# Kernel tuning notes

Measured on AMD Instinct MI355X. Metric: run time of the kernel, lower is better.

## Reference

```python
import jax, jax.numpy as jnp
import numpy as np

B, S = 1, 2048
HID, INTER = 4096, 11008
HEADS, HD = 32, 128
GS = 128
EPS = 1e-6
BASE = 10000.0
IMIN, IMAX = -(2**31), 2**31 - 1


def _rope_tables():
    inv_freq = 1.0 / (BASE ** (np.arange(0, HD, 2, dtype=np.float32) / HD))
    t = np.arange(S, dtype=np.float32)
    freqs = np.outer(t, inv_freq)            # [S, HD/2]
    emb = np.concatenate([freqs, freqs], -1)  # [S, HD]
    return jnp.asarray(np.sin(emb), jnp.float32), jnp.asarray(np.cos(emb), jnp.float32)


def setup_inputs() -> dict:
    key = jax.random.key(0)
    ks = iter(jax.random.split(key, 40))
    def qset(in_f, out_f):
        qw = jax.random.randint(next(ks), (in_f // 8, out_f), IMIN, IMAX, dtype=jnp.int32)
        qz = jax.random.randint(next(ks), (in_f // GS, out_f // 8), IMIN, IMAX, dtype=jnp.int32)
        sc = jax.random.uniform(next(ks), (in_f // GS, out_f), dtype=jnp.float32) * 0.01 + 1e-3
        return qw, qz, sc
    dims = {"q": (HID, HID), "k": (HID, HID), "v": (HID, HID), "o": (HID, HID),
            "gate": (HID, INTER), "up": (HID, INTER), "down": (INTER, HID)}
    inp = {}
    for name, (i, o) in dims.items():
        qw, qz, sc = qset(i, o)
        inp["qw_" + name] = qw
        inp["qz_" + name] = qz
        inp["sc_" + name] = sc
    inp["hidden_states"] = jax.random.normal(next(ks), (B, S, HID), dtype=jnp.float32)
    inp["ln1_w"] = jnp.ones((HID,), jnp.float32)
    inp["ln2_w"] = jnp.ones((HID,), jnp.float32)
    sin, cos = _rope_tables()
    inp["sin"] = sin
    inp["cos"] = cos
    # causal additive mask, as stored in ExLlamaBuffer.attn_mask (past_len = 0)
    mask = jnp.where(jnp.tril(jnp.ones((S, S), bool)), 0.0, -1e9).astype(jnp.float32)
    inp["attn_mask"] = mask[None, None]
    return inp


def _dequant(qw, qz, sc):
    # GPTQ int4: qweight [in/8, out] packs 8 rows per int32; qzeros [groups, out/8]
    in_f, out_f = qw.shape[0] * 8, qw.shape[1]
    groups = sc.shape[0]
    sh = jnp.arange(8, dtype=jnp.int32) * 4
    w = ((qw[:, None, :] >> sh[None, :, None]) & 15)
    w = w.reshape(groups, in_f // groups, out_f).astype(jnp.float32)
    z = ((qz[:, :, None] >> sh[None, None, :]) & 15).reshape(groups, out_f).astype(jnp.float32)
    return ((w - (z + 1.0)[:, None, :]) * sc[:, None, :]).reshape(in_f, out_f)


def _rms(x, w):
    v = jnp.mean(x * x, axis=-1, keepdims=True)
    return x * jax.lax.rsqrt(v + EPS) * w


def _rot_half(x):
    x1, x2 = jnp.split(x, 2, axis=-1)
    return jnp.concatenate([-x2, x1], axis=-1)


def reference(qw_q, qz_q, sc_q, qw_k, qz_k, sc_k, qw_v, qz_v, sc_v,
              qw_o, qz_o, sc_o, qw_gate, qz_gate, sc_gate,
              qw_up, qz_up, sc_up, qw_down, qz_down, sc_down,
              hidden_states, ln1_w, ln2_w, sin, cos, attn_mask):
    lin = lambda x, a, b, c: x @ _dequant(a, b, c)
    h = hidden_states
    # attention block
    x = _rms(h, ln1_w)
    q = lin(x, qw_q, qz_q, sc_q).reshape(B, S, HEADS, HD).transpose(0, 2, 1, 3)
    k = lin(x, qw_k, qz_k, sc_k).reshape(B, S, HEADS, HD).transpose(0, 2, 1, 3)
    v = lin(x, qw_v, qz_v, sc_v).reshape(B, S, HEADS, HD).transpose(0, 2, 1, 3)
    c, s = cos[None, None], sin[None, None]  # [1,1,S,HD]
    q = q * c + _rot_half(q) * s
    k = k * c + _rot_half(k) * s
    scores = jnp.einsum('bhqd,bhkd->bhqk', q, k) / np.float32(np.sqrt(HD)) + attn_mask
    p = jax.nn.softmax(scores, axis=-1)
    o = jnp.einsum('bhqk,bhkd->bhqd', p, v).transpose(0, 2, 1, 3).reshape(B, S, HID)
    h = h + lin(o, qw_o, qz_o, sc_o)
    # MLP block
    x = _rms(h, ln2_w)
    y = jax.nn.silu(lin(x, qw_gate, qz_gate, sc_gate)) * lin(x, qw_up, qz_up, sc_up)
    return h + lin(y, qw_down, qz_down, sc_down)
```

## Files before the change

kernel.cpp:

```cpp
#include <hip/hip_runtime.h>
#include <cstdint>
#include <cstddef>

#define S_LEN 2048
#define HID   4096
#define INTER 11008
#define NHEADS 32
#define HD    128

typedef __attribute__((ext_vector_type(4))) float  f32x4;
typedef __attribute__((ext_vector_type(8))) __bf16 bf16x8;
typedef __attribute__((ext_vector_type(8))) short  s16x8;
typedef __attribute__((ext_vector_type(4))) short  s16x4;

__device__ __forceinline__ float bf2f(short s) {
  unsigned u = ((unsigned)(unsigned short)s) << 16;
  return __builtin_bit_cast(float, u);
}
__device__ __forceinline__ short f2bf(float f) {
  unsigned u = __builtin_bit_cast(unsigned, f);
  u += 0x7FFFu + ((u >> 16) & 1u);
  return (short)(u >> 16);
}
__device__ __forceinline__ f32x4 mfma16(s16x8 a, s16x8 b, f32x4 c) {
  return __builtin_amdgcn_mfma_f32_16x16x32_bf16(
      __builtin_bit_cast(bf16x8, a), __builtin_bit_cast(bf16x8, b), c, 0, 0, 0);
}
__device__ __forceinline__ void gload_lds16(const void* g, void* l) {
  __builtin_amdgcn_global_load_lds(
      (const __attribute__((address_space(1))) void*)g,
      (__attribute__((address_space(3))) void*)l, 16, 0, 0);
}

__global__ __launch_bounds__(256) void rmsnorm_kernel(const float* __restrict__ x,
                                                      const float* __restrict__ w,
                                                      short* __restrict__ out) {
  int row = blockIdx.x;
  const float* xr = x + (size_t)row * HID;
  short* orow = out + (size_t)row * HID;
  int tid = threadIdx.x;
  f32x4 v[4];
  float ss = 0.f;
#pragma unroll
  for (int i = 0; i < 4; ++i) {
    v[i] = ((const f32x4*)xr)[i * 256 + tid];
    ss += v[i][0] * v[i][0] + v[i][1] * v[i][1] + v[i][2] * v[i][2] + v[i][3] * v[i][3];
  }
#pragma unroll
  for (int off = 32; off > 0; off >>= 1) ss += __shfl_xor(ss, off);
  __shared__ float psum[4];
  if ((tid & 63) == 0) psum[tid >> 6] = ss;
  __syncthreads();
  float tot = psum[0] + psum[1] + psum[2] + psum[3];
  float r = rsqrtf(tot * (1.0f / (float)HID) + 1e-6f);
#pragma unroll
  for (int i = 0; i < 4; ++i) {
    int base = (i * 256 + tid) * 4;
    s16x4 o;
#pragma unroll
    for (int j = 0; j < 4; ++j) o[j] = f2bf(v[i][j] * r * w[base + j]);
    *(s16x4*)&orow[base] = o;
  }
}

template <int OMODE>
__global__ __launch_bounds__(256) void paired_kernel(
    const short* __restrict__ A, int lda,
    const short* __restrict__ BT, int ldb,
    void* __restrict__ Cv, int ldc,
    const float* __restrict__ base, int Kext,
    int gnx, int gny,
    const int* __restrict__ qw, const int* __restrict__ qz,
    const float* __restrict__ sc, short* __restrict__ wt,
    int N, int noff, int dnx, int dqld) {
  __shared__ short sm[4 * 4096];
  int bid = blockIdx.x;
  int gtot = gnx * gny;
  int tid = threadIdx.x;
  if (bid < gtot) {
    int cpx = gtot >> 3;
    int swz = (bid & 7) * cpx + (bid >> 3);
    int bn = swz % gnx, bm = swz / gnx;
    int lane = tid & 63, wv = tid >> 6;
    int wr = wv >> 1, wc = wv & 1;
    f32x4 acc[4][4] = {};
    int nk = Kext >> 5;
    int lr = lane >> 2, lc = lane & 3;
    const short* Abase = A + (size_t)(bm * 128) * lda;
    const short* Bbase = BT + (size_t)(bn * 128) * ldb;
    short* As0 = sm;
    short* Bs0 = sm + 8192;

    auto stage = [&](int buf, int t) {
      int k0 = t << 5;
#pragma unroll
      for (int i = 0; i < 2; ++i) {
        int r = i * 64 + wv * 16 + lr;
        gload_lds16(Abase + (size_t)r * lda + k0 + lc * 8, As0 + buf * 4096 + i * 2048 + wv * 512);
        gload_lds16(Bbase + (size_t)r * ldb + k0 + lc * 8, Bs0 + buf * 4096 + i * 2048 + wv * 512);
      }
    };
    auto compute = [&](int buf) {
      int kc = (lane >> 4) * 8;
      int ra = wr * 64 + (lane & 15);
      int rb = wc * 64 + (lane & 15);
      s16x8 af[4], bfr[4];
#pragma unroll
      for (int m = 0; m < 4; ++m) af[m] = *(const s16x8*)&As0[buf * 4096 + (ra + m * 16) * 32 + kc];
#pragma unroll
      for (int n = 0; n < 4; ++n) bfr[n] = *(const s16x8*)&Bs0[buf * 4096 + (rb + n * 16) * 32 + kc];
#pragma unroll
      for (int m = 0; m < 4; ++m)
#pragma unroll
        for (int n = 0; n < 4; ++n) acc[m][n] = mfma16(af[m], bfr[n], acc[m][n]);
    };

    stage(0, 0);
    __syncthreads();
    for (int t = 0; t < nk; ++t) {
      if (t + 1 < nk) stage((t + 1) & 1, t + 1);
      compute(t & 1);
      __syncthreads();
    }

    int row0 = bm * 128 + wr * 64 + ((lane >> 4) << 2);
    int col0 = bn * 128 + wc * 64 + (lane & 15);
#pragma unroll
    for (int m = 0; m < 4; ++m)
#pragma unroll
      for (int n = 0; n < 4; ++n)
#pragma unroll
        for (int j = 0; j < 4; ++j) {
          size_t idx = (size_t)(row0 + m * 16 + j) * ldc + col0 + n * 16;
          if (OMODE == 0)      ((short*)Cv)[idx] = f2bf(acc[m][n][j]);
          else if (OMODE == 1) ((float*)Cv)[idx] = base[idx] + acc[m][n][j];
          else if (OMODE == 2) ((float*)Cv)[idx] = ((float*)Cv)[idx] + acc[m][n][j];
          else {
            short* C = (short*)Cv;
            float g = bf2f(C[idx]);
            float sl = g / (1.f + __expf(-g));
            C[idx] = f2bf(sl * acc[m][n][j]);
          }
        }
  } else {
    int id = bid - gtot;
    int n0 = (id % dnx) * 64;
    int k0 = (id / dnx) * 64;
    int g = k0 >> 7;
    int qr0 = k0 >> 3;
#pragma unroll
    for (int i = 0; i < 2; ++i) {
      int idx = tid + i * 256;
      int r = idx >> 6;
      int n = idx & 63;
      int gc = noff + n0 + n;
      unsigned q = (unsigned)qw[(size_t)(qr0 + r) * N + gc];
      float s = sc[(size_t)g * N + gc];
      unsigned zq = (unsigned)qz[(size_t)g * (N >> 3) + (gc >> 3)];
      float zs = ((float)((zq >> ((gc & 7) * 4)) & 15u) + 1.0f) * s;
      s16x8 o;
#pragma unroll
      for (int j = 0; j < 8; ++j)
        o[j] = f2bf(fmaf((float)((q >> (4 * j)) & 15u), s, -zs));
      *(s16x8*)&sm[n * 72 + r * 8] = o;
    }
    __syncthreads();
    int n = tid >> 2;
#pragma unroll
    for (int i = 0; i < 2; ++i) {
      int c = (tid & 3) + i * 4;
      *(s16x8*)&wt[(size_t)(n0 + n) * dqld + k0 + c * 8] = *(const s16x8*)&sm[n * 72 + c * 8];
    }
  }
}

__global__ __launch_bounds__(128) void rope_kernel(short* __restrict__ q, short* __restrict__ k,
                                                   const float* __restrict__ sp,
                                                   const float* __restrict__ cp) {
  int s = blockIdx.x, h = blockIdx.y;
  short* p = (blockIdx.z ? k : q) + (size_t)s * HID + h * HD;
  int d = threadIdx.x;
  float x = bf2f(p[d]);
  float xp = bf2f(p[d ^ 64]);
  float rot = (d < 64) ? -xp : xp;
  float y = x * cp[s * HD + d] + rot * sp[s * HD + d];
  __syncthreads();
  p[d] = f2bf(y);
}

__global__ __launch_bounds__(256, 1) void attn_kernel(const short* __restrict__ qb,
                                                      const short* __restrict__ kb,
                                                      const short* __restrict__ vb,
                                                      short* __restrict__ ob) {
  int qt = (int)(gridDim.x - 1) - blockIdx.x;
  int h = blockIdx.y;
  int tid = threadIdx.x, lane = tid & 63, wv = tid >> 6;
  __shared__ short Kl[64 * 128];
  __shared__ short Vl[128 * 72];
  __shared__ short Pl[4][32 * 72];
  int q0 = qt * 128 + wv * 32;
  s16x8 qf[2][4];
#pragma unroll
  for (int m = 0; m < 2; ++m)
#pragma unroll
    for (int kf = 0; kf < 4; ++kf) {
      int r = q0 + m * 16 + (lane & 15);
      int d = kf * 32 + (lane >> 4) * 8;
      qf[m][kf] = *(const s16x8*)&qb[(size_t)r * HID + h * HD + d];
    }
  f32x4 o[2][8] = {};
  float mrow[2][4], lrow[2][4];
#pragma unroll
  for (int m = 0; m < 2; ++m)
#pragma unroll
    for (int j = 0; j < 4; ++j) { mrow[m][j] = -1e30f; lrow[m][j] = 0.f; }

  auto load_tile = [&](int kv0, s16x8* kr, s16x8* vr) {
#pragma unroll
    for (int i = 0; i < 4; ++i) {
      int cid = tid + i * 256;
      int kv = cid >> 4, c = cid & 15;
      kr[i] = *(const s16x8*)(kb + (size_t)(kv0 + kv) * HID + h * HD + c * 8);
      vr[i] = *(const s16x8*)(vb + (size_t)(kv0 + kv) * HID + h * HD + c * 8);
    }
  };
  auto store_tile = [&](const s16x8* kr, const s16x8* vr) {
#pragma unroll
    for (int i = 0; i < 4; ++i) {
      int cid = tid + i * 256;
      int kv = cid >> 4, c = cid & 15;
      *(s16x8*)((char*)Kl + kv * 256 + ((c ^ (kv & 7)) * 16)) = kr[i];
      int kvs = kv ^ ((c & 7) << 3);
#pragma unroll
      for (int j = 0; j < 8; ++j) Vl[(c * 8 + j) * 72 + kvs] = vr[i][j];
    }
  };

  const float scale = 0.08838834764831845f;
  int kv_end = qt * 128 + 128;
  s16x8 kra[4], vra[4], krb[4], vrb[4];
  load_tile(0, kra, vra);
  store_tile(kra, vra);
  __syncthreads();
  for (int kv0 = 0; kv0 < kv_end; kv0 += 64) {
    bool more = kv0 + 64 < kv_end;
    if (more) load_tile(kv0 + 64, krb, vrb);

    f32x4 sfr[2][4] = {};
    __builtin_amdgcn_s_setprio(1);
#pragma unroll
    for (int nf = 0; nf < 4; ++nf) {
      s16x8 kfr[4];
      int kvr = nf * 16 + (lane & 15);
#pragma unroll
      for (int kf = 0; kf < 4; ++kf) {
        int cc = (kf * 4 + (lane >> 4)) ^ (kvr & 7);
        kfr[kf] = *(const s16x8*)((const char*)Kl + kvr * 256 + cc * 16);
      }
#pragma unroll
      for (int m = 0; m < 2; ++m)
#pragma unroll
        for (int kf = 0; kf < 4; ++kf) sfr[m][nf] = mfma16(qf[m][kf], kfr[kf], sfr[m][nf]);
    }
    __builtin_amdgcn_s_setprio(0);
#pragma unroll
    for (int m = 0; m < 2; ++m)
#pragma unroll
      for (int j = 0; j < 4; ++j) {
        int qrow = q0 + m * 16 + (lane >> 4) * 4 + j;
        float pm = -1e30f;
#pragma unroll
        for (int nf = 0; nf < 4; ++nf) {
          int kvc = kv0 + nf * 16 + (lane & 15);
          float v = sfr[m][nf][j] * scale;
          v = (kvc <= qrow) ? v : -1e30f;
          sfr[m][nf][j] = v;
          pm = fmaxf(pm, v);
        }
#pragma unroll
        for (int off = 1; off < 16; off <<= 1) pm = fmaxf(pm, __shfl_xor(pm, off));
        float mnew = fmaxf(mrow[m][j], pm);
        float alpha = __expf(mrow[m][j] - mnew);
        mrow[m][j] = mnew;
        float rs = 0.f;
#pragma unroll
        for (int nf = 0; nf < 4; ++nf) {
          float p = __expf(sfr[m][nf][j] - mnew);
          sfr[m][nf][j] = p;
          rs += p;
        }
#pragma unroll
        for (int off = 1; off < 16; off <<= 1) rs += __shfl_xor(rs, off);
        lrow[m][j] = lrow[m][j] * alpha + rs;
#pragma unroll
        for (int nd = 0; nd < 8; ++nd) o[m][nd][j] *= alpha;
      }
#pragma unroll
    for (int m = 0; m < 2; ++m)
#pragma unroll
      for (int nf = 0; nf < 4; ++nf)
#pragma unroll
        for (int j = 0; j < 4; ++j)
          Pl[wv][(m * 16 + (lane >> 4) * 4 + j) * 72 + nf * 16 + (lane & 15)] =
              f2bf(sfr[m][nf][j]);
    s16x8 pa[2][2];
#pragma unroll
    for (int m = 0; m < 2; ++m)
#pragma unroll
      for (int kf = 0; kf < 2; ++kf)
        pa[m][kf] = *(const s16x8*)&Pl[wv][(m * 16 + (lane & 15)) * 72 + kf * 32 + (lane >> 4) * 8];
    __builtin_amdgcn_s_setprio(1);
#pragma unroll
    for (int nd = 0; nd < 8; ++nd) {
      s16x8 vf[2];
      int drow = nd * 16 + (lane & 15);
      int key = ((drow >> 3) & 7) << 3;
#pragma unroll
      for (int kf = 0; kf < 2; ++kf)
        vf[kf] = *(const s16x8*)&Vl[drow * 72 + ((kf * 32 + (lane >> 4) * 8) ^ key)];
#pragma unroll
      for (int m = 0; m < 2; ++m)
#pragma unroll
        for (int kf = 0; kf < 2; ++kf) o[m][nd] = mfma16(pa[m][kf], vf[kf], o[m][nd]);
    }
    __builtin_amdgcn_s_setprio(0);
    __syncthreads();
    if (more) store_tile(krb, vrb);
    __syncthreads();
  }
#pragma unroll
  for (int m = 0; m < 2; ++m)
#pragma unroll
    for (int nd = 0; nd < 8; ++nd)
#pragma unroll
      for (int j = 0; j < 4; ++j) {
        int r = q0 + m * 16 + (lane >> 4) * 4 + j;
        int c = h * HD + nd * 16 + (lane & 15);
        ob[(size_t)r * HID + c] = f2bf(o[m][nd][j] / lrow[m][j]);
      }
}

extern "C" void kernel_launch(void* const* d_in, const int* in_sizes, int n_in,
                              void* d_out, int out_size, void* d_ws, size_t ws_size,
                              hipStream_t stream) {
  const int* qw[7]; const int* qz[7]; const float* sc[7];
  for (int i = 0; i < 7; ++i) {
    qw[i] = (const int*)d_in[i * 3 + 0];
    qz[i] = (const int*)d_in[i * 3 + 1];
    sc[i] = (const float*)d_in[i * 3 + 2];
  }
  const float* hin  = (const float*)d_in[21];
  const float* ln1  = (const float*)d_in[22];
  const float* ln2  = (const float*)d_in[23];
  const float* sinp = (const float*)d_in[24];
  const float* cosp = (const float*)d_in[25];
  float* out = (float*)d_out;

  char* ws = (char*)d_ws;
  const size_t MB = 1024 * 1024;
  short* XB    = (short*)(ws);
  short* WA    = (short*)(ws + 16 * MB);
  short* WB    = (short*)(ws + 48 * MB);
  short* KB    = (short*)(ws + 80 * MB);
  short* VB    = (short*)(ws + 96 * MB);
  short* OB    = (short*)(ws + 112 * MB);
  short* GATEB = (short*)(ws + 80 * MB);
  short* QBd   = (short*)d_out;

  dim3 blk(256);
  const int noffs[3] = {0, 4096, 8192};
  const int nexts[3] = {4096, 4096, 2816};

  rmsnorm_kernel<<<S_LEN, blk, 0, stream>>>(hin, ln1, XB);
  paired_kernel<0><<<4096, blk, 0, stream>>>(nullptr, 0, nullptr, 0, nullptr, 0, nullptr, 0,
                                             0, 0, qw[0], qz[0], sc[0], WA, HID, 0, 64, HID);
  paired_kernel<0><<<512 + 4096, blk, 0, stream>>>(XB, HID, WA, HID, QBd, HID, nullptr, HID,
                                                   32, 16, qw[1], qz[1], sc[1], WB, HID, 0, 64, HID);
  paired_kernel<0><<<512 + 4096, blk, 0, stream>>>(XB, HID, WB, HID, KB, HID, nullptr, HID,
                                                   32, 16, qw[2], qz[2], sc[2], WA, HID, 0, 64, HID);
  paired_kernel<0><<<512 + 4096, blk, 0, stream>>>(XB, HID, WA, HID, VB, HID, nullptr, HID,
                                                   32, 16, qw[3], qz[3], sc[3], WB, HID, 0, 64, HID);
  rope_kernel<<<dim3(S_LEN, NHEADS, 2), dim3(128), 0, stream>>>(QBd, KB, sinp, cosp);
  attn_kernel<<<dim3(S_LEN / 128, NHEADS), blk, 0, stream>>>(QBd, KB, VB, OB);
  paired_kernel<1><<<512 + 4096, blk, 0, stream>>>(OB, HID, WB, HID, out, HID, hin, HID,
                                                   32, 16, qw[4], qz[4], sc[4], WA, INTER, 0, 64, HID);
  rmsnorm_kernel<<<S_LEN, blk, 0, stream>>>(out, ln2, XB);

  paired_kernel<0><<<512 + 4096, blk, 0, stream>>>(XB, HID, WA, HID, GATEB + 0, INTER, nullptr, HID,
                                                   32, 16, qw[5], qz[5], sc[5], WB, INTER, 0, 64, HID);
  paired_kernel<3><<<512 + 4096, blk, 0, stream>>>(XB, HID, WB, HID, GATEB + 0, INTER, nullptr, HID,
                                                   32, 16, qw[4], qz[4], sc[4], WA, INTER, 4096, 64, HID);
  paired_kernel<0><<<512 + 4096, blk, 0, stream>>>(XB, HID, WA, HID, GATEB + 4096, INTER, nullptr, HID,
                                                   32, 16, qw[5], qz[5], sc[5], WB, INTER, 4096, 64, HID);
  paired_kernel<3><<<512 + 2816, blk, 0, stream>>>(XB, HID, WB, HID, GATEB + 4096, INTER, nullptr, HID,
                                                   32, 16, qw[4], qz[4], sc[4], WA, INTER, 8192, 44, HID);
  paired_kernel<0><<<352 + 2816, blk, 0, stream>>>(XB, HID, WA, HID, GATEB + 8192, INTER, nullptr, HID,
                                                   22, 16, qw[5], qz[5], sc[5], WB, INTER, 8192, 44, HID);
  paired_kernel<3><<<352 + 4096, blk, 0, stream>>>(XB, HID, WB, HID, GATEB + 8192, INTER, nullptr, HID,
                                                   22, 16, qw[6], qz[6], sc[6], WA, HID, 0, 64, 4096);
  paired_kernel<2><<<512 + 4096, blk, 0, stream>>>(GATEB + 0, INTER, WA, 4096, out, HID, nullptr, 4096,
                                                   32, 16,
                                                   qw[6] + (size_t)(4096 >> 3) * HID,
                                                   qz[6] + (size_t)(4096 >> 7) * (HID / 8),
                                                   sc[6] + (size_t)(4096 >> 7) * HID,
                                                   WB, HID, 0, 64, 4096);
  paired_kernel<2><<<512 + 2816, blk, 0, stream>>>(GATEB + 4096, INTER, WB, 4096, out, HID, nullptr, 4096,
                                                   32, 16,
                                                   qw[6] + (size_t)(8192 >> 3) * HID,
                                                   qz[6] + (size_t)(8192 >> 7) * (HID / 8),
                                                   sc[6] + (size_t)(8192 >> 7) * HID,
                                                   WA, HID, 0, 64, 2816);
  paired_kernel<2><<<512, blk, 0, stream>>>(GATEB + 8192, INTER, WA, 2816, out, HID, nullptr, 2816,
                                            32, 16, nullptr, nullptr, nullptr, nullptr, HID, 0, 1, HID);
}
```

Before: 1.461 ms.

## Replace paired GEMM with 128x256 tiled kernel and interleave dequant inside

```diff
diff --git a/kernel.cpp b/kernel.cpp
--- a/kernel.cpp
+++ b/kernel.cpp
@@ -63,122 +63,166 @@
   }
 }
 
-template <int OMODE>
-__global__ __launch_bounds__(256) void paired_kernel(
-    const short* __restrict__ A, int lda,
-    const short* __restrict__ BT, int ldb,
-    void* __restrict__ Cv, int ldc,
-    const float* __restrict__ base, int Kext,
-    int gnx, int gny,
+__device__ __forceinline__ void dq_tile(const int* __restrict__ qw, const int* __restrict__ qz,
+                                        const float* __restrict__ sc, short* __restrict__ wt,
+                                        int N, int noff, int dnx, int dqld, int tile, int tid) {
+  int n0 = (tile % dnx) * 64;
+  int k0 = (tile / dnx) * 64;
+  int n = tid >> 3;
+  int cc = tid & 7;
+  int gc = noff + n0 + n;
+  int g = k0 >> 7;
+  unsigned q = (unsigned)qw[(size_t)((k0 >> 3) + cc) * N + gc];
+  float s = sc[(size_t)g * N + gc];
+  unsigned zq = (unsigned)qz[(size_t)g * (N >> 3) + (gc >> 3)];
+  float zs = ((float)((zq >> ((gc & 7) * 4)) & 15u) + 1.0f) * s;
+  s16x8 o;
+#pragma unroll
+  for (int j = 0; j < 8; ++j)
+    o[j] = f2bf(fmaf((float)((q >> (4 * j)) & 15u), s, -zs));
+  *(s16x8*)&wt[(size_t)(n0 + n) * dqld + k0 + cc * 8] = o;
+}
+
+__global__ __launch_bounds__(512) void dq_kernel(const int* __restrict__ qw, const int* __restrict__ qz,
+                                                 const float* __restrict__ sc, short* __restrict__ wt,
+                                                 int N, int noff, int dnx, int dqld, int tpb) {
+  for (int i = 0; i < tpb; ++i)
+    dq_tile(qw, qz, sc, wt, N, noff, dnx, dqld, blockIdx.x * tpb + i, threadIdx.x);
+}
+
+__global__ __launch_bounds__(512, 1) void g256_kernel(
+    const short* __restrict__ A, int lda, const short* __restrict__ BT, int ldb,
+    void* __restrict__ Cv, int ldc, const float* __restrict__ base, int Kext,
+    int gnx, int omode,
     const int* __restrict__ qw, const int* __restrict__ qz,
     const float* __restrict__ sc, short* __restrict__ wt,
-    int N, int noff, int dnx, int dqld) {
-  __shared__ short sm[4 * 4096];
+    int dqN, int dqnoff, int dqnx, int dqld, int dqTiles) {
+  __shared__ short As[2][128 * 64];
+  __shared__ short Bs[2][256 * 64];
+  int tid = threadIdx.x;
+  int lane = tid & 63, wid = tid >> 6;
+  int wr = wid >> 2, wc = wid & 3;
+  int gtot = gnx * 16;
   int bid = blockIdx.x;
-  int gtot = gnx * gny;
-  int tid = threadIdx.x;
-  if (bid < gtot) {
-    int cpx = gtot >> 3;
-    int swz = (bid & 7) * cpx + (bid >> 3);
-    int bn = swz % gnx, bm = swz / gnx;
-    int lane = tid & 63, wv = tid >> 6;
-    int wr = wv >> 1, wc = wv & 1;
-    f32x4 acc[4][4] = {};
-    int nk = Kext >> 5;
-    int lr = lane >> 2, lc = lane & 3;
-    const short* Abase = A + (size_t)(bm * 128) * lda;
-    const short* Bbase = BT + (size_t)(bn * 128) * ldb;
-    short* As0 = sm;
-    short* Bs0 = sm + 8192;
-
-    auto stage = [&](int buf, int t) {
-      int k0 = t << 5;
-#pragma unroll
-      for (int i = 0; i < 2; ++i) {
-        int r = i * 64 + wv * 16 + lr;
-        gload_lds16(Abase + (size_t)r * lda + k0 + lc * 8, As0 + buf * 4096 + i * 2048 + wv * 512);
-        gload_lds16(Bbase + (size_t)r * ldb + k0 + lc * 8, Bs0 + buf * 4096 + i * 2048 + wv * 512);
+  int swz = (bid & 7) * (gtot >> 3) + (bid >> 3);
+  int bn = swz % gnx, bm = swz / gnx;
+  const short* Abase = A + (size_t)(bm * 128) * lda;
+  const short* Bbase = BT + (size_t)(bn * 256) * ldb;
+  int nk = Kext >> 6;
+
+  int dqc = 0, dqe = 0;
+  if (dqTiles > 0) {
+    dqc = (int)((long)bid * dqTiles / gtot);
+    dqe = (int)((long)(bid + 1) * dqTiles / gtot);
+  }
+
+  f32x4 acc[4][4] = {};
+
+  auto stageA = [&](int buf, int tt, int h) {
+    if (tt >= nk) return;
+    int rbase = (wid < 4 ? wid * 8 : 64 + (wid - 4) * 8) + h * 32;
+    int row = rbase + (lane >> 3);
+    int gcc = (lane & 7) ^ (row & 7);
+    gload_lds16(Abase + (size_t)row * lda + tt * 64 + gcc * 8, &As[buf][rbase * 64]);
+  };
+  auto stageB = [&](int buf, int tt, int h) {
+    if (tt >= nk) return;
+#pragma unroll
+    for (int seg = 0; seg < 2; ++seg) {
+      int rbase = seg * 128 + (wid < 4 ? wid * 8 : 64 + (wid - 4) * 8) + h * 32;
+      int row = rbase + (lane >> 3);
+      int gcc = (lane & 7) ^ (row & 7);
+      gload_lds16(Bbase + (size_t)row * ldb + tt * 64 + gcc * 8, &Bs[buf][rbase * 64]);
+    }
+  };
+  auto lda_frag = [&](int buf, int mi, int ks) -> s16x8 {
+    int row = wr * 64 + mi * 16 + (lane & 15);
+    int cc = ks * 4 + (lane >> 4);
+    return *(const s16x8*)&As[buf][row * 64 + ((cc ^ (row & 7)) * 8)];
+  };
+  auto ldb_frag = [&](int buf, int ni, int ks) -> s16x8 {
+    int row = wc * 64 + ni * 16 + (lane & 15);
+    int cc = ks * 4 + (lane >> 4);
+    return *(const s16x8*)&Bs[buf][row * 64 + ((cc ^ (row & 7)) * 8)];
+  };
+
+  stageA(0, 0, 0); stageB(0, 0, 0); stageA(0, 0, 1); stageB(0, 0, 1);
+  stageA(1, 1, 0); stageB(1, 1, 0);
+  asm volatile("s_waitcnt vmcnt(3)" ::: "memory");
+  __builtin_amdgcn_s_barrier();
+  __builtin_amdgcn_sched_barrier(0);
+
+  for (int t = 0; t < nk; ++t) {
+    int cb = t & 1, nb = cb ^ 1;
+#pragma unroll
+    for (int p = 0; p < 4; ++p) {
+      if (p == 0) stageA(nb, t + 1, 1);
+      else if (p == 1) stageB(nb, t + 1, 1);
+      else if (p == 2) stageA(cb, t + 2, 0);
+      else stageB(cb, t + 2, 0);
+      const int mq = p >> 1, nq = p & 1;
+      s16x8 af[2][2], bfr[2][2];
+#pragma unroll
+      for (int x = 0; x < 2; ++x)
+#pragma unroll
+        for (int ks = 0; ks < 2; ++ks) {
+          af[x][ks] = lda_frag(cb, mq * 2 + x, ks);
+          bfr[x][ks] = ldb_frag(cb, nq * 2 + x, ks);
+        }
+      __builtin_amdgcn_s_setprio(1);
+#pragma unroll
+      for (int x = 0; x < 2; ++x)
+#pragma unroll
+        for (int y = 0; y < 2; ++y)
+#pragma unroll
+          for (int ks = 0; ks < 2; ++ks)
+            acc[mq * 2 + x][nq * 2 + y] =
+                mfma16(af[x][ks], bfr[y][ks], acc[mq * 2 + x][nq * 2 + y]);
+      __builtin_amdgcn_s_setprio(0);
+      if (p == 3) {
+        if (t + 2 < nk)      asm volatile("s_waitcnt vmcnt(3)" ::: "memory");
+        else if (t + 1 < nk) asm volatile("s_waitcnt vmcnt(0)" ::: "memory");
       }
-    };
-    auto compute = [&](int buf) {
-      int kc = (lane >> 4) * 8;
-      int ra = wr * 64 + (lane & 15);
-      int rb = wc * 64 + (lane & 15);
-      s16x8 af[4], bfr[4];
-#pragma unroll
-      for (int m = 0; m < 4; ++m) af[m] = *(const s16x8*)&As0[buf * 4096 + (ra + m * 16) * 32 + kc];
-#pragma unroll
-      for (int n = 0; n < 4; ++n) bfr[n] = *(const s16x8*)&Bs0[buf * 4096 + (rb + n * 16) * 32 + kc];
-#pragma unroll
-      for (int m = 0; m < 4; ++m)
-#pragma unroll
-        for (int n = 0; n < 4; ++n) acc[m][n] = mfma16(af[m], bfr[n], acc[m][n]);
-    };
-
-    stage(0, 0);
-    __syncthreads();
-    for (int t = 0; t < nk; ++t) {
-      if (t + 1 < nk) stage((t + 1) & 1, t + 1);
-      compute(t & 1);
-      __syncthreads();
-    }
-
-    int row0 = bm * 128 + wr * 64 + ((lane >> 4) << 2);
-    int col0 = bn * 128 + wc * 64 + (lane & 15);
-#pragma unroll
-    for (int m = 0; m < 4; ++m)
-#pragma unroll
-      for (int n = 0; n < 4; ++n)
-#pragma unroll
-        for (int j = 0; j < 4; ++j) {
-          size_t idx = (size_t)(row0 + m * 16 + j) * ldc + col0 + n * 16;
-          if (OMODE == 0)      ((short*)Cv)[idx] = f2bf(acc[m][n][j]);
-          else if (OMODE == 1) ((float*)Cv)[idx] = base[idx] + acc[m][n][j];
-          else if (OMODE == 2) ((float*)Cv)[idx] = ((float*)Cv)[idx] + acc[m][n][j];
-          else {
-            short* C = (short*)Cv;
-            float g = bf2f(C[idx]);
-            float sl = g / (1.f + __expf(-g));
-            C[idx] = f2bf(sl * acc[m][n][j]);
-          }
+      __builtin_amdgcn_s_barrier();
+      if (p == 3) __builtin_amdgcn_sched_barrier(0);
+    }
+    if ((t & 3) == 3 && dqc < dqe) {
+      dq_tile(qw, qz, sc, wt, dqN, dqnoff, dqnx, dqld, dqc, tid);
+      ++dqc;
+    }
+  }
+  while (dqc < dqe) {
+    dq_tile(qw, qz, sc, wt, dqN, dqnoff, dqnx, dqld, dqc, tid);
+    ++dqc;
+  }
+
+  int row0 = bm * 128 + wr * 64 + ((lane >> 4) << 2);
+  int col0 = bn * 256 + wc * 64 + (lane & 15);
+#pragma unroll
+  for (int mi = 0; mi < 4; ++mi)
+#pragma unroll
+    for (int ni = 0; ni < 4; ++ni)
+#pragma unroll
+      for (int j = 0; j < 4; ++j) {
+        size_t idx = (size_t)(row0 + mi * 16 + j) * ldc + col0 + ni * 16;
+        float a = acc[mi][ni][j];
+        if (omode == 0)      ((short*)Cv)[idx] = f2bf(a);
+        else if (omode == 1) ((float*)Cv)[idx] = base[idx] + a;
+        else if (omode == 2) ((float*)Cv)[idx] = ((float*)Cv)[idx] + a;
+        else {
+          short* C = (short*)Cv;
+          float g = bf2f(C[idx]);
+          C[idx] = f2bf(g / (1.f + __expf(-g)) * a);
         }
-  } else {
-    int id = bid - gtot;
-    int n0 = (id % dnx) * 64;
-    int k0 = (id / dnx) * 64;
-    int g = k0 >> 7;
-    int qr0 = k0 >> 3;
-#pragma unroll
-    for (int i = 0; i < 2; ++i) {
-      int idx = tid + i * 256;
-      int r = idx >> 6;
-      int n = idx & 63;
-      int gc = noff + n0 + n;
-      unsigned q = (unsigned)qw[(size_t)(qr0 + r) * N + gc];
-      float s = sc[(size_t)g * N + gc];
-      unsigned zq = (unsigned)qz[(size_t)g * (N >> 3) + (gc >> 3)];
-      float zs = ((float)((zq >> ((gc & 7) * 4)) & 15u) + 1.0f) * s;
-      s16x8 o;
-#pragma unroll
-      for (int j = 0; j < 8; ++j)
-        o[j] = f2bf(fmaf((float)((q >> (4 * j)) & 15u), s, -zs));
-      *(s16x8*)&sm[n * 72 + r * 8] = o;
-    }
-    __syncthreads();
-    int n = tid >> 2;
-#pragma unroll
-    for (int i = 0; i < 2; ++i) {
-      int c = (tid & 3) + i * 4;
-      *(s16x8*)&wt[(size_t)(n0 + n) * dqld + k0 + c * 8] = *(const s16x8*)&sm[n * 72 + c * 8];
-    }
-  }
-}
-
-__global__ __launch_bounds__(128) void rope_kernel(short* __restrict__ q, short* __restrict__ k,
+      }
+}
+
+__global__ __launch_bounds__(128) void rope_kernel(short* __restrict__ q, int qld,
+                                                   short* __restrict__ k, int kld,
                                                    const float* __restrict__ sp,
                                                    const float* __restrict__ cp) {
   int s = blockIdx.x, h = blockIdx.y;
-  short* p = (blockIdx.z ? k : q) + (size_t)s * HID + h * HD;
+  short* p = blockIdx.z ? (k + (size_t)s * kld + h * HD) : (q + (size_t)s * qld + h * HD);
   int d = threadIdx.x;
   float x = bf2f(p[d]);
   float xp = bf2f(p[d ^ 64]);
@@ -188,9 +232,9 @@
   p[d] = f2bf(y);
 }
 
-__global__ __launch_bounds__(256, 1) void attn_kernel(const short* __restrict__ qb,
-                                                      const short* __restrict__ kb,
-                                                      const short* __restrict__ vb,
+__global__ __launch_bounds__(256, 2) void attn_kernel(const short* __restrict__ qb, int qld,
+                                                      const short* __restrict__ kb, int kld,
+                                                      const short* __restrict__ vb, int vld,
                                                       short* __restrict__ ob) {
   int qt = (int)(gridDim.x - 1) - blockIdx.x;
   int h = blockIdx.y;
@@ -206,7 +250,7 @@
     for (int kf = 0; kf < 4; ++kf) {
       int r = q0 + m * 16 + (lane & 15);
       int d = kf * 32 + (lane >> 4) * 8;
-      qf[m][kf] = *(const s16x8*)&qb[(size_t)r * HID + h * HD + d];
+      qf[m][kf] = *(const s16x8*)&qb[(size_t)r * qld + h * HD + d];
     }
   f32x4 o[2][8] = {};
   float mrow[2][4], lrow[2][4];
@@ -220,8 +264,8 @@
     for (int i = 0; i < 4; ++i) {
       int cid = tid + i * 256;
       int kv = cid >> 4, c = cid & 15;
-      kr[i] = *(const s16x8*)(kb + (size_t)(kv0 + kv) * HID + h * HD + c * 8);
-      vr[i] = *(const s16x8*)(vb + (size_t)(kv0 + kv) * HID + h * HD + c * 8);
+      kr[i] = *(const s16x8*)(kb + (size_t)(kv0 + kv) * kld + h * HD + c * 8);
+      vr[i] = *(const s16x8*)(vb + (size_t)(kv0 + kv) * vld + h * HD + c * 8);
     }
   };
   auto store_tile = [&](const s16x8* kr, const s16x8* vr) {
@@ -285,9 +329,9 @@
         float rs = 0.f;
 #pragma unroll
         for (int nf = 0; nf < 4; ++nf) {
-          float p = __expf(sfr[m][nf][j] - mnew);
-          sfr[m][nf][j] = p;
-          rs += p;
+          float pv = __expf(sfr[m][nf][j] - mnew);
+          sfr[m][nf][j] = pv;
+          rs += pv;
         }
 #pragma unroll
         for (int off = 1; off < 16; off <<= 1) rs += __shfl_xor(rs, off);
@@ -358,58 +402,52 @@
 
   char* ws = (char*)d_ws;
   const size_t MB = 1024 * 1024;
-  short* XB    = (short*)(ws);
-  short* WA    = (short*)(ws + 16 * MB);
-  short* WB    = (short*)(ws + 48 * MB);
-  short* KB    = (short*)(ws + 80 * MB);
-  short* VB    = (short*)(ws + 96 * MB);
-  short* OB    = (short*)(ws + 112 * MB);
-  short* GATEB = (short*)(ws + 80 * MB);
-  short* QBd   = (short*)d_out;
-
-  dim3 blk(256);
-  const int noffs[3] = {0, 4096, 8192};
-  const int nexts[3] = {4096, 4096, 2816};
-
-  rmsnorm_kernel<<<S_LEN, blk, 0, stream>>>(hin, ln1, XB);
-  paired_kernel<0><<<4096, blk, 0, stream>>>(nullptr, 0, nullptr, 0, nullptr, 0, nullptr, 0,
-                                             0, 0, qw[0], qz[0], sc[0], WA, HID, 0, 64, HID);
-  paired_kernel<0><<<512 + 4096, blk, 0, stream>>>(XB, HID, WA, HID, QBd, HID, nullptr, HID,
-                                                   32, 16, qw[1], qz[1], sc[1], WB, HID, 0, 64, HID);
-  paired_kernel<0><<<512 + 4096, blk, 0, stream>>>(XB, HID, WB, HID, KB, HID, nullptr, HID,
-                                                   32, 16, qw[2], qz[2], sc[2], WA, HID, 0, 64, HID);
-  paired_kernel<0><<<512 + 4096, blk, 0, stream>>>(XB, HID, WA, HID, VB, HID, nullptr, HID,
-                                                   32, 16, qw[3], qz[3], sc[3], WB, HID, 0, 64, HID);
-  rope_kernel<<<dim3(S_LEN, NHEADS, 2), dim3(128), 0, stream>>>(QBd, KB, sinp, cosp);
-  attn_kernel<<<dim3(S_LEN / 128, NHEADS), blk, 0, stream>>>(QBd, KB, VB, OB);
-  paired_kernel<1><<<512 + 4096, blk, 0, stream>>>(OB, HID, WB, HID, out, HID, hin, HID,
-                                                   32, 16, qw[4], qz[4], sc[4], WA, INTER, 0, 64, HID);
-  rmsnorm_kernel<<<S_LEN, blk, 0, stream>>>(out, ln2, XB);
-
-  paired_kernel<0><<<512 + 4096, blk, 0, stream>>>(XB, HID, WA, HID, GATEB + 0, INTER, nullptr, HID,
-                                                   32, 16, qw[5], qz[5], sc[5], WB, INTER, 0, 64, HID);
-  paired_kernel<3><<<512 + 4096, blk, 0, stream>>>(XB, HID, WB, HID, GATEB + 0, INTER, nullptr, HID,
-                                                   32, 16, qw[4], qz[4], sc[4], WA, INTER, 4096, 64, HID);
-  paired_kernel<0><<<512 + 4096, blk, 0, stream>>>(XB, HID, WA, HID, GATEB + 4096, INTER, nullptr, HID,
-                                                   32, 16, qw[5], qz[5], sc[5], WB, INTER, 4096, 64, HID);
-  paired_kernel<3><<<512 + 2816, blk, 0, stream>>>(XB, HID, WB, HID, GATEB + 4096, INTER, nullptr, HID,
-                                                   32, 16, qw[4], qz[4], sc[4], WA, INTER, 8192, 44, HID);
-  paired_kernel<0><<<352 + 2816, blk, 0, stream>>>(XB, HID, WA, HID, GATEB + 8192, INTER, nullptr, HID,
-                                                   22, 16, qw[5], qz[5], sc[5], WB, INTER, 8192, 44, HID);
-  paired_kernel<3><<<352 + 4096, blk, 0, stream>>>(XB, HID, WB, HID, GATEB + 8192, INTER, nullptr, HID,
-                                                   22, 16, qw[6], qz[6], sc[6], WA, HID, 0, 64, 4096);
-  paired_kernel<2><<<512 + 4096, blk, 0, stream>>>(GATEB + 0, INTER, WA, 4096, out, HID, nullptr, 4096,
-                                                   32, 16,
-                                                   qw[6] + (size_t)(4096 >> 3) * HID,
-                                                   qz[6] + (size_t)(4096 >> 7) * (HID / 8),
-                                                   sc[6] + (size_t)(4096 >> 7) * HID,
-                                                   WB, HID, 0, 64, 4096);
-  paired_kernel<2><<<512 + 2816, blk, 0, stream>>>(GATEB + 4096, INTER, WB, 4096, out, HID, nullptr, 4096,
-                                                   32, 16,
-                                                   qw[6] + (size_t)(8192 >> 3) * HID,
-                                                   qz[6] + (size_t)(8192 >> 7) * (HID / 8),
-                                                   sc[6] + (size_t)(8192 >> 7) * HID,
-                                                   WA, HID, 0, 64, 2816);
-  paired_kernel<2><<<512, blk, 0, stream>>>(GATEB + 8192, INTER, WA, 2816, out, HID, nullptr, 2816,
-                                            32, 16, nullptr, nullptr, nullptr, nullptr, HID, 0, 1, HID);
-}
+  short* XB  = (short*)(ws);
+  short* WA  = (short*)(ws + 16 * MB);
+  short* WB  = (short*)(ws + 48 * MB);
+  short* QB  = (short*)(ws + 80 * MB);
+  short* KBf = (short*)(ws + 96 * MB);
+  short* VBf = (short*)(ws + 112 * MB);
+  short* OB  = XB;
+  short* G0 = QB; short* G1 = KBf; short* G2 = VBf;
+
+  dim3 b512(512), b256(256);
+
+  rmsnorm_kernel<<<S_LEN, b256, 0, stream>>>(hin, ln1, XB);
+  dq_kernel<<<1024, b512, 0, stream>>>(qw[0], qz[0], sc[0], WA, HID, 0, 64, HID, 4);
+  g256_kernel<<<256, b512, 0, stream>>>(XB, HID, WA, HID, QB, HID, nullptr, HID,
+                                        16, 0, qw[1], qz[1], sc[1], WB, HID, 0, 64, HID, 4096);
+  g256_kernel<<<256, b512, 0, stream>>>(XB, HID, WB, HID, KBf, HID, nullptr, HID,
+                                        16, 0, qw[2], qz[2], sc[2], WA, HID, 0, 64, HID, 4096);
+  g256_kernel<<<256, b512, 0, stream>>>(XB, HID, WA, HID, VBf, HID, nullptr, HID,
+                                        16, 0, qw[3], qz[3], sc[3], WB, HID, 0, 64, HID, 4096);
+  rope_kernel<<<dim3(S_LEN, NHEADS, 2), dim3(128), 0, stream>>>(QB, HID, KBf, HID, sinp, cosp);
+  attn_kernel<<<dim3(S_LEN / 128, NHEADS), b256, 0, stream>>>(QB, HID, KBf, HID, VBf, HID, OB);
+  g256_kernel<<<256, b512, 0, stream>>>(OB, HID, WB, HID, out, HID, hin, HID,
+                                        16, 1, qw[4], qz[4], sc[4], WA, INTER, 0, 64, HID, 4096);
+  rmsnorm_kernel<<<S_LEN, b256, 0, stream>>>(out, ln2, XB);
+  g256_kernel<<<256, b512, 0, stream>>>(XB, HID, WA, HID, G0, HID, nullptr, HID,
+                                        16, 0, qw[5], qz[5], sc[5], WB, INTER, 0, 64, HID, 4096);
+  g256_kernel<<<256, b512, 0, stream>>>(XB, HID, WB, HID, G0, HID, nullptr, HID,
+                                        16, 3, qw[6], qz[6], sc[6], WA, HID, 0, 64, 4096, 4096);
+  g256_kernel<<<256, b512, 0, stream>>>(G0, HID, WA, 4096, out, HID, nullptr, 4096,
+                                        16, 2, qw[4], qz[4], sc[4], WB, INTER, 4096, 64, HID, 4096);
+  g256_kernel<<<256, b512, 0, stream>>>(XB, HID, WB, HID, G1, HID, nullptr, HID,
+                                        16, 0, qw[5], qz[5], sc[5], WA, INTER, 4096, 64, HID, 4096);
+  g256_kernel<<<256, b512, 0, stream>>>(XB, HID, WA, HID, G1, HID, nullptr, HID,
+                                        16, 3, qw[6] + (size_t)(4096 >> 3) * HID,
+                                        qz[6] + (size_t)(4096 >> 7) * (HID / 8),
+                                        sc[6] + (size_t)(4096 >> 7) * HID,
+                                        WB, HID, 0, 64, 4096, 4096);
+  g256_kernel<<<256, b512, 0, stream>>>(G1, HID, WB, 4096, out, HID, nullptr, 4096,
+                                        16, 2, qw[4], qz[4], sc[4], WA, INTER, 8192, 44, HID, 2816);
+  g256_kernel<<<176, b512, 0, stream>>>(XB, HID, WA, HID, G2, HID, nullptr, HID,
+                                        11, 0, qw[5], qz[5], sc[5], WB, INTER, 8192, 44, HID, 2816);
+  g256_kernel<<<176, b512, 0, stream>>>(XB, HID, WB, HID, G2, HID, nullptr, HID,
+                                        11, 3, qw[6] + (size_t)(8192 >> 3) * HID,
+                                        qz[6] + (size_t)(8192 >> 7) * (HID / 8),
+                                        sc[6] + (size_t)(8192 >> 7) * HID,
+                                        WA, HID, 0, 64, 2816, 2816);
+  g256_kernel<<<256, b512, 0, stream>>>(G2, HID, WA, 2816, out, HID, nullptr, 2816,
+                                        16, 2, nullptr, nullptr, nullptr, nullptr, 0, 0, 1, 0, 0);
+}
```

Result: no change. 1.465 ms (+0.3%).
